# Optimization experiments

Hardware: AMD Instinct MI355X
Metric: run time of the kernel (lower is better)

The kernel has to match this reference:

```python
import jax, jax.numpy as jnp
import numpy as np

B, T, D, H, L, VOC = 2, 2048, 512, 8, 4, 32000
SLOTS = [16384, 8192, 4096]  # base_slots=16384, halved per level
KTOP = 4


def setup_inputs() -> dict:
    key = jax.random.key(0)
    ks = jax.random.split(key, 20)

    def n(i, shape, scale=0.02):
        return jax.random.normal(ks[i], shape, jnp.float32) * scale

    inp = {
        'input_ids': jax.random.randint(ks[0], (B, T), 0, VOC),
        'tok_embed': n(1, (VOC, D)),
        'pos_embed': n(2, (T, D)),
        'Wqkv': n(3, (L, 3 * D, D)), 'bqkv': jnp.zeros((L, 3 * D), jnp.float32),
        'Wo': n(4, (L, D, D)), 'bo': jnp.zeros((L, D), jnp.float32),
        'ln1_s': jnp.ones((L, D), jnp.float32), 'ln1_b': jnp.zeros((L, D), jnp.float32),
        'W1': n(5, (L, 4 * D, D)), 'b1': jnp.zeros((L, 4 * D), jnp.float32),
        'W2': n(6, (L, D, 4 * D)), 'b2': jnp.zeros((L, D), jnp.float32),
        'ln2_s': jnp.ones((L, D), jnp.float32), 'ln2_b': jnp.zeros((L, D), jnp.float32),
        'Wq': n(7, (D, D)), 'bq': jnp.zeros((D,), jnp.float32),
        'Wrp': n(8, (D, D)), 'brp': jnp.zeros((D,), jnp.float32),
        'lnout_s': jnp.ones((D,), jnp.float32), 'lnout_b': jnp.zeros((D,), jnp.float32),
    }
    # hierarchical memory banks (xavier-ish scale)
    for li, s in enumerate(SLOTS):
        inp[f'K{li}'] = n(10 + li, (s, D), float(1.0 / np.sqrt(D)))
        inp[f'V{li}'] = n(13 + li, (s, D), float(1.0 / np.sqrt(D)))
        inp[f's{li}'] = jnp.zeros((s,), jnp.float32)
    return inp


def _ln(x, s, b):
    m = x.mean(-1, keepdims=True)
    v = jnp.mean((x - m) ** 2, -1, keepdims=True)
    return (x - m) / jnp.sqrt(v + 1e-5) * s + b


def reference(input_ids, tok_embed, pos_embed, Wqkv, bqkv, Wo, bo, ln1_s, ln1_b,
              W1, b1, W2, b2, ln2_s, ln2_b, Wq, bq, Wrp, brp, lnout_s, lnout_b,
              K0, V0, s0, K1, V1, s1, K2, V2, s2):
    hd = D // H
    x = tok_embed[input_ids] + pos_embed[None, :, :]  # [B,T,D]
    for i in range(L):
        qkv = x @ Wqkv[i].T + bqkv[i]
        q, k, v = jnp.split(qkv, 3, -1)
        q = q.reshape(B, T, H, hd)
        k = k.reshape(B, T, H, hd)
        v = v.reshape(B, T, H, hd)
        att = jax.nn.softmax(jnp.einsum('bqhd,bkhd->bhqk', q, k) / np.float32(np.sqrt(hd)), -1)
        o = jnp.einsum('bhqk,bkhd->bqhd', att, v).reshape(B, T, D)
        x = _ln(x + (o @ Wo[i].T + bo[i]), ln1_s[i], ln1_b[i])
        f = jax.nn.gelu(x @ W1[i].T + b1[i], approximate=False) @ W2[i].T + b2[i]
        x = _ln(x + f, ln2_s[i], ln2_b[i])
    # hierarchical memory read (top-k gather attention per level)
    qm = x @ Wq.T + bq
    inv_sqrt_d = np.float32(1.0 / np.sqrt(D))
    read = jnp.zeros_like(x)
    for (K, V, sal) in ((K0, V0, s0), (K1, V1, s1), (K2, V2, s2)):
        scores = jnp.einsum('btd,sd->bts', qm, K) * inv_sqrt_d + sal  # [B,T,S]
        ts, ti = jax.lax.top_k(scores, KTOP)
        a = jax.nn.softmax(ts, -1)                 # [B,T,k]
        read = read + jnp.einsum('btk,btkd->btd', a, V[ti])  # gather + reduce
    read = read / np.float32(len(SLOTS))           # uniform level weights 1/num_levels
    x = x + (read @ Wrp.T + brp)
    x = _ln(x, lnout_s, lnout_b)
    return x @ tok_embed.T                          # tied lm_head [B,T,VOC]
```

## Files before the change

### kernel.cpp

```cpp
#include <hip/hip_runtime.h>
#include <cstdint>

typedef __bf16 bf16_t;
typedef __bf16 bf16x2 __attribute__((ext_vector_type(2)));
typedef __bf16 bf16x4 __attribute__((ext_vector_type(4)));
typedef __bf16 bf16x8 __attribute__((ext_vector_type(8)));
typedef float f32x4 __attribute__((ext_vector_type(4)));
typedef unsigned short u16;
typedef unsigned int u32;
typedef unsigned short u16x8 __attribute__((ext_vector_type(8)));

#define DEVI static __device__ __forceinline__

DEVI void g2l16(const void* g, void* l) {
  __builtin_amdgcn_global_load_lds((__attribute__((address_space(1))) void*)g,
                                   (__attribute__((address_space(3))) void*)l,
                                   16, 0, 0);
}

DEVI void tki4(u32* k, u32 nk) {
  if (nk <= k[3]) return;
  k[3] = nk;
  if (k[3] > k[2]) { u32 t = k[2]; k[2] = k[3]; k[3] = t; }
  if (k[2] > k[1]) { u32 t = k[1]; k[1] = k[2]; k[2] = t; }
  if (k[1] > k[0]) { u32 t = k[0]; k[0] = k[1]; k[1] = t; }
}

struct F2BArgs {
  const float* s[10];
  bf16_t* d[10];
  int n4[10];
};
__global__ void k_f2b_all(F2BArgs a) {
  const int seg = blockIdx.y;
  const float* __restrict__ in = a.s[seg];
  bf16_t* __restrict__ out = a.d[seg];
  const long n4 = a.n4[seg];
  const long stride = (long)gridDim.x * blockDim.x;
  for (long i = (long)blockIdx.x * blockDim.x + threadIdx.x; i < n4; i += stride) {
    float4 v = ((const float4*)in)[i];
    bf16x4 o = {(bf16_t)v.x, (bf16_t)v.y, (bf16_t)v.z, (bf16_t)v.w};
    ((bf16x4*)out)[i] = o;
  }
}

__global__ void k_embed(const int* __restrict__ ids, const float* __restrict__ tok,
                        const float* __restrict__ pos, float* __restrict__ x,
                        bf16_t* __restrict__ xb) {
  int r = blockIdx.x;
  int t = r & 2047;
  long id = ids[r];
  int d = threadIdx.x * 2;
  float2 a = *(const float2*)(tok + id * 512 + d);
  float2 p = *(const float2*)(pos + (long)t * 512 + d);
  float o0 = a.x + p.x, o1 = a.y + p.y;
  *(float2*)(x + (long)r * 512 + d) = make_float2(o0, o1);
  bf16x2 ob = {(bf16_t)o0, (bf16_t)o1};
  *(bf16x2*)(xb + (long)r * 512 + d) = ob;
}

DEVI float gelu_f(float f) {
  return 0.5f * f * (1.0f + erff(f * 0.70710678118654752f));
}

template <typename CT, bool BIAS, int EPI>
__global__ __launch_bounds__(256, 2) void k_gemm_bt(
    const bf16_t* __restrict__ A, int lda, const bf16_t* __restrict__ B, int ldb,
    CT* __restrict__ C, int ldc, const float* __restrict__ bias, int K, float alpha,
    bf16_t* __restrict__ qh, bf16_t* __restrict__ kh, bf16_t* __restrict__ vt) {
  __shared__ bf16_t As[4096];
  __shared__ bf16_t Bs[4096];
  const int tid = threadIdx.x;
  const int lane = tid & 63;
  const int w = tid >> 6;
  const int wm = w >> 1, wn = w & 1;
  const int m0 = blockIdx.y * 128;
  const int n0 = blockIdx.x * 128;

  f32x4 acc[4][4];
#pragma unroll
  for (int m = 0; m < 4; ++m)
#pragma unroll
    for (int n = 0; n < 4; ++n) acc[m][n] = (f32x4){0.f, 0.f, 0.f, 0.f};

  const int srow = tid >> 2;
  const int scol = ((tid & 3) ^ ((srow >> 1) & 3)) * 8;
  const int fr = lane & 15;
  const int g4 = lane >> 4;
  const int kg = g4 * 8;

  for (int k0 = 0; k0 < K; k0 += 32) {
#pragma unroll
    for (int p = 0; p < 2; ++p) {
      g2l16(A + (long long)(m0 + p * 64 + srow) * lda + (k0 + scol), As + p * 2048 + w * 512);
      g2l16(B + (long long)(n0 + p * 64 + srow) * ldb + (k0 + scol), Bs + p * 2048 + w * 512);
    }
    __syncthreads();
    bf16x8 fa[4], fb[4];
#pragma unroll
    for (int m = 0; m < 4; ++m) {
      const int row = wm * 64 + m * 16 + fr;
      fa[m] = *(const bf16x8*)(As + row * 32 + (kg ^ (((row >> 1) & 3) << 3)));
    }
#pragma unroll
    for (int n = 0; n < 4; ++n) {
      const int row = wn * 64 + n * 16 + fr;
      fb[n] = *(const bf16x8*)(Bs + row * 32 + (kg ^ (((row >> 1) & 3) << 3)));
    }
#pragma unroll
    for (int m = 0; m < 4; ++m)
#pragma unroll
      for (int n = 0; n < 4; ++n)
        acc[m][n] = __builtin_amdgcn_mfma_f32_16x16x32_bf16(fa[m], fb[n], acc[m][n], 0, 0, 0);
    __syncthreads();
  }

#pragma unroll
  for (int n = 0; n < 4; ++n) {
    const int col = n0 + wn * 64 + n * 16 + fr;
    const float bv = BIAS ? bias[col] : 0.0f;
    if (EPI == 1) {
      const int reg = col >> 9;
      const int h = (col >> 6) & 7;
      const int hd = col & 63;
#pragma unroll
      for (int m = 0; m < 4; ++m) {
        const int rb = m0 + wm * 64 + m * 16 + g4 * 4;
#pragma unroll
        for (int r = 0; r < 4; ++r) {
          const int row = rb + r;
          const int b = row >> 11, t = row & 2047;
          const long long bh = (long long)b * 8 + h;
          float v = acc[m][n][r] + bv;
          if (reg == 0) qh[(bh * 2048 + t) * 64 + hd] = (bf16_t)(v * 0.125f);
          else if (reg == 1) kh[(bh * 2048 + t) * 64 + hd] = (bf16_t)v;
          else vt[(bh * 64 + hd) * 2048 + t] = (bf16_t)v;
        }
      }
    } else {
#pragma unroll
      for (int m = 0; m < 4; ++m) {
        const long long rb = m0 + wm * 64 + m * 16 + g4 * 4;
#pragma unroll
        for (int r = 0; r < 4; ++r) {
          float v = (acc[m][n][r] + bv) * alpha;
          if (EPI == 2) v = gelu_f(v);
          C[(rb + r) * (long long)ldc + col] = (CT)v;
        }
      }
    }
  }
}

template <typename CT, bool BIAS>
__global__ __launch_bounds__(256, 4) void k_gemm64(
    const bf16_t* __restrict__ A, int lda, const bf16_t* __restrict__ B, int ldb,
    CT* __restrict__ C, int ldc, long long sCz, const float* __restrict__ bias,
    int K, float alpha) {
  __shared__ bf16_t As[64 * 32];
  __shared__ bf16_t Bs[128 * 32];
  const int tid = threadIdx.x;
  const int lane = tid & 63;
  const int w = tid >> 6;
  const int wm = w >> 1, wn = w & 1;
  const int m0 = blockIdx.y * 64;
  const int n0 = blockIdx.x * 128;
  const int kz = blockIdx.z;
  A += (long long)kz * K;
  B += (long long)kz * K;
  C += (long long)kz * sCz;

  f32x4 acc[2][4];
#pragma unroll
  for (int m = 0; m < 2; ++m)
#pragma unroll
    for (int n = 0; n < 4; ++n) acc[m][n] = (f32x4){0.f, 0.f, 0.f, 0.f};

  const int srow = tid >> 2;
  const int scol = ((tid & 3) ^ ((srow >> 1) & 3)) * 8;
  const int fr = lane & 15;
  const int g4 = lane >> 4;
  const int kg = g4 * 8;

  for (int k0 = 0; k0 < K; k0 += 32) {
    g2l16(A + (long long)(m0 + srow) * lda + (k0 + scol), As + tid * 8);
    g2l16(B + (long long)(n0 + srow) * ldb + (k0 + scol), Bs + tid * 8);
    g2l16(B + (long long)(n0 + 64 + srow) * ldb + (k0 + scol), Bs + 2048 + tid * 8);
    __syncthreads();
    bf16x8 fa[2], fb[4];
#pragma unroll
    for (int m = 0; m < 2; ++m) {
      const int row = wm * 32 + m * 16 + fr;
      fa[m] = *(const bf16x8*)(As + row * 32 + (kg ^ (((row >> 1) & 3) << 3)));
    }
#pragma unroll
    for (int n = 0; n < 4; ++n) {
      const int row = wn * 64 + n * 16 + fr;
      fb[n] = *(const bf16x8*)(Bs + row * 32 + (kg ^ (((row >> 1) & 3) << 3)));
    }
#pragma unroll
    for (int m = 0; m < 2; ++m)
#pragma unroll
      for (int n = 0; n < 4; ++n)
        acc[m][n] = __builtin_amdgcn_mfma_f32_16x16x32_bf16(fa[m], fb[n], acc[m][n], 0, 0, 0);
    __syncthreads();
  }

#pragma unroll
  for (int n = 0; n < 4; ++n) {
    const int col = n0 + wn * 64 + n * 16 + fr;
    const float bv = (BIAS && kz == 0) ? bias[col] : 0.0f;
#pragma unroll
    for (int m = 0; m < 2; ++m) {
      const long long rb = m0 + wm * 32 + m * 16 + g4 * 4;
#pragma unroll
      for (int r = 0; r < 4; ++r)
        C[(rb + r) * (long long)ldc + col] = (CT)((acc[m][n][r] + bv) * alpha);
    }
  }
}

template <typename CT, int EPI>
__global__ __launch_bounds__(512, 2) void k_gemm256(
    const bf16_t* __restrict__ A, int lda, const bf16_t* __restrict__ B, int ldb,
    CT* __restrict__ C, int ldc, int K, float alpha,
    const float* __restrict__ s0, const float* __restrict__ s1,
    const float* __restrict__ s2, u32* __restrict__ cand) {
  __shared__ char lds[131072];
  const int tid = threadIdx.x;
  const int lane = tid & 63;
  const int w = tid >> 6;
  const int wm = w >> 2, wn = w & 3;
  const int fr = lane & 15;
  const int g4 = lane >> 4;

  const int ny = gridDim.y;
  const int nwg = gridDim.x * ny;
  int orig = blockIdx.y * gridDim.x + blockIdx.x;
  int lin = ((nwg & 7) == 0) ? ((orig & 7) * (nwg >> 3) + (orig >> 3)) : orig;
  const int m0 = (lin % ny) * 256;
  const int n0 = (lin / ny) * 256;

  f32x4 acc[8][4];
#pragma unroll
  for (int m = 0; m < 8; ++m)
#pragma unroll
    for (int n = 0; n < 4; ++n) acc[m][n] = (f32x4){0.f, 0.f, 0.f, 0.f};

  const int sr = tid >> 2;
  const int sc = (tid & 3) * 16;
  const int NT = K >> 6;

  auto stage = [&](int t, int p, int buf) {
    const long long kb = (long long)t * 128 + p * 64;
    char* ab = (char*)lds + buf * 65536 + p * 16384;
    char* bb = ab + 32768;
    const int sw = ((sr >> 1) & 3) << 4;
    g2l16((const char*)A + (long long)(m0 + sr) * (lda * 2) + kb + (sc ^ sw), ab + tid * 16);
    g2l16((const char*)A + (long long)(m0 + 128 + sr) * (lda * 2) + kb + (sc ^ sw),
          ab + (tid + 512) * 16);
    g2l16((const char*)B + (long long)(n0 + sr) * (ldb * 2) + kb + (sc ^ sw), bb + tid * 16);
    g2l16((const char*)B + (long long)(n0 + 128 + sr) * (ldb * 2) + kb + (sc ^ sw),
          bb + (tid + 512) * 16);
  };

  stage(0, 0, 0);
  stage(0, 1, 0);
  asm volatile("s_waitcnt vmcnt(4)" ::: "memory");
  __builtin_amdgcn_s_barrier();
  __builtin_amdgcn_sched_barrier(0);

  int cur = 0;
  for (int t = 0; t < NT; ++t) {
#pragma unroll
    for (int p = 0; p < 2; ++p) {
      const char* ab = (const char*)lds + cur * 65536 + p * 16384;
      const char* bb = ab + 32768;
      bf16x8 fa[8], fb[4];
#pragma unroll
      for (int m = 0; m < 8; ++m) {
        const int row = wm * 128 + m * 16 + fr;
        fa[m] = *(const bf16x8*)(ab + row * 64 + ((g4 * 16) ^ (((row >> 1) & 3) << 4)));
      }
#pragma unroll
      for (int n = 0; n < 4; ++n) {
        const int row = wn * 64 + n * 16 + fr;
        fb[n] = *(const bf16x8*)(bb + row * 64 + ((g4 * 16) ^ (((row >> 1) & 3) << 4)));
      }
      if (t + 1 < NT) stage(t + 1, p, cur ^ 1);
      if (t == NT - 1 && p == 0) {
        asm volatile("s_waitcnt vmcnt(0)" ::: "memory");
      } else {
        asm volatile("s_waitcnt vmcnt(4)" ::: "memory");
      }
      __builtin_amdgcn_s_barrier();
      __builtin_amdgcn_sched_barrier(0);
      __builtin_amdgcn_s_setprio(1);
#pragma unroll
      for (int m = 0; m < 8; ++m)
#pragma unroll
        for (int n = 0; n < 4; ++n)
          acc[m][n] = __builtin_amdgcn_mfma_f32_16x16x32_bf16(fa[m], fb[n], acc[m][n], 0, 0, 0);
      __builtin_amdgcn_s_setprio(0);
    }
    cur ^= 1;
  }

  if (EPI == 0) {
#pragma unroll
    for (int n = 0; n < 4; ++n) {
      const int col = n0 + wn * 64 + n * 16 + fr;
#pragma unroll
      for (int m = 0; m < 8; ++m) {
        const long long rb = m0 + wm * 128 + m * 16 + g4 * 4;
#pragma unroll
        for (int r = 0; r < 4; ++r)
          C[(rb + r) * (long long)ldc + col] = (CT)(acc[m][n][r] * alpha);
      }
    }
  } else {
    const float* salp;
    if (n0 < 16384) salp = s0 + n0;
    else if (n0 < 24576) salp = s1 + (n0 - 16384);
    else salp = s2 + (n0 - 24576);
    float bv[4];
    int coll[4];
#pragma unroll
    for (int n = 0; n < 4; ++n) {
      coll[n] = wn * 64 + n * 16 + fr;
      bv[n] = salp[coll[n]];
    }
    __syncthreads();
    u16* slab = (u16*)lds;
#pragma unroll
    for (int m = 0; m < 8; ++m) {
#pragma unroll
      for (int r = 0; r < 4; ++r) {
        const int rl = wm * 128 + m * 16 + g4 * 4 + r;
        const int sw = (rl & 7) << 3;
#pragma unroll
        for (int n = 0; n < 4; ++n) {
          bf16_t bvv = (bf16_t)(acc[m][n][r] + bv[n]);
          slab[rl * 256 + (coll[n] ^ sw)] = __builtin_bit_cast(u16, bvv);
        }
      }
    }
    __syncthreads();
    const int rr = tid & 255;
    const int hh = tid >> 8;
    const int sw = (rr & 7) << 3;
    u32 rk[4] = {0u, 0u, 0u, 0u};
    const u32 ibase = 0x7FFFu - (u32)n0;
#pragma unroll
    for (int j = 0; j < 16; ++j) {
      const int c0 = hh * 128 + j * 8;
      u16x8 vv = *(const u16x8*)(slab + rr * 256 + (c0 ^ sw));
#pragma unroll
      for (int e = 0; e < 8; ++e) {
        u16 sb = vv[e];
        u32 k16 = (u32)sb ^ (0x8000u | (0x7FFFu * (u32)(sb >> 15)));
        tki4(rk, (k16 << 15) | (ibase - (u32)(c0 + e)));
      }
    }
    __syncthreads();
    u32* res = (u32*)lds;
#pragma unroll
    for (int j = 0; j < 4; ++j) res[(rr * 2 + hh) * 4 + j] = rk[j];
    __syncthreads();
    if (tid < 256) {
      const u32* rp = res + tid * 8;
      u32 fin[4] = {rp[0], rp[1], rp[2], rp[3]};
      tki4(fin, rp[4]); tki4(fin, rp[5]); tki4(fin, rp[6]); tki4(fin, rp[7]);
      u32* cp = cand + ((long long)(m0 + tid) * 112 + (n0 >> 8)) * 4;
#pragma unroll
      for (int j = 0; j < 4; ++j) cp[j] = fin[j];
    }
  }
}

__global__ __launch_bounds__(256, 2) void k_flash(
    const bf16_t* __restrict__ qh, const bf16_t* __restrict__ kh,
    const bf16_t* __restrict__ vt, bf16_t* __restrict__ out) {
  __shared__ bf16_t Ks[2][128 * 64];
  __shared__ bf16_t Vs[2][64 * 128];
  __shared__ bf16_t Ps[4 * 16 * 128];
  const int tid = threadIdx.x;
  const int lane = tid & 63;
  const int w = tid >> 6;
  const int bh = blockIdx.y;
  const int q0 = blockIdx.x * 64;
  const int fr = lane & 15;
  const int g4 = lane >> 4;
  const int kg = g4 * 8;

  bf16x8 qf[2];
  {
    const bf16_t* qb = qh + ((long long)bh * 2048 + q0 + w * 16) * 64;
#pragma unroll
    for (int ks = 0; ks < 2; ++ks)
      qf[ks] = *(const bf16x8*)(qb + fr * 64 + ks * 32 + kg);
  }

  f32x4 oacc[4];
#pragma unroll
  for (int n = 0; n < 4; ++n) oacc[n] = (f32x4){0.f, 0.f, 0.f, 0.f};
  float li[4] = {0.f, 0.f, 0.f, 0.f};

  char* PsW = (char*)(Ps + w * 16 * 128);
  const bf16_t* kbase = kh + (long long)bh * 2048 * 64;
  const bf16_t* vbase = vt + (long long)bh * 64 * 2048;

  auto stage = [&](int kt, int buf) {
#pragma unroll
    for (int i = 0; i < 4; ++i) {
      int row = (w * 4 + i) * 8 + (lane >> 3);
      int c = lane & 7;
      g2l16(kbase + ((long long)(kt * 128 + row)) * 64 + (c ^ (row & 7)) * 8,
            Ks[buf] + (w * 4 + i) * 512);
      int d = w * 16 + i * 4 + (lane >> 4);
      int c2 = lane & 15;
      g2l16(vbase + (long long)d * 2048 + kt * 128 + ((c2 ^ (d & 7)) * 8),
            Vs[buf] + (w * 16 + i * 4) * 128);
    }
  };

  stage(0, 0);
  int buf = 0;
  for (int kt = 0; kt < 16; ++kt) {
    __syncthreads();
    if (kt + 1 < 16) stage(kt + 1, buf ^ 1);

    f32x4 s[8];
#pragma unroll
    for (int n = 0; n < 8; ++n) s[n] = (f32x4){0.f, 0.f, 0.f, 0.f};
#pragma unroll
    for (int ks = 0; ks < 2; ++ks) {
#pragma unroll
      for (int n = 0; n < 8; ++n) {
        int row = n * 16 + fr;
        bf16x8 kf = *(const bf16x8*)((const char*)Ks[buf] + row * 128 +
                                     ((ks * 64 + kg * 2) ^ ((row & 7) << 4)));
        s[n] = __builtin_amdgcn_mfma_f32_16x16x32_bf16(qf[ks], kf, s[n], 0, 0, 0);
      }
    }

#pragma unroll
    for (int r = 0; r < 4; ++r) {
      const int lr = g4 * 4 + r;
      const int sw = (lr & 7) << 4;
      float rs = 0.f;
#pragma unroll
      for (int n = 0; n < 8; ++n) {
        float p = __expf(s[n][r]);
        rs += p;
        *(bf16_t*)(PsW + lr * 256 + (((n * 16 + fr) * 2) ^ sw)) = (bf16_t)p;
      }
      li[r] += rs;
    }

#pragma unroll
    for (int ks = 0; ks < 4; ++ks) {
      bf16x8 pa = *(const bf16x8*)(PsW + fr * 256 +
                                   ((ks * 64 + kg * 2) ^ ((fr & 7) << 4)));
#pragma unroll
      for (int n = 0; n < 4; ++n) {
        int d = n * 16 + fr;
        bf16x8 vf = *(const bf16x8*)((const char*)Vs[buf] + d * 256 +
                                     ((ks * 64 + kg * 2) ^ ((d & 7) << 4)));
        oacc[n] = __builtin_amdgcn_mfma_f32_16x16x32_bf16(pa, vf, oacc[n], 0, 0, 0);
      }
    }
    buf ^= 1;
  }

#pragma unroll
  for (int r = 0; r < 4; ++r) {
    li[r] += __shfl_xor(li[r], 1);
    li[r] += __shfl_xor(li[r], 2);
    li[r] += __shfl_xor(li[r], 4);
    li[r] += __shfl_xor(li[r], 8);
  }

  const int b = bh >> 3, h = bh & 7;
  bf16_t* ob = out + ((long long)b * 2048 + q0 + w * 16) * 512 + h * 64;
#pragma unroll
  for (int r = 0; r < 4; ++r) {
    float inv = 1.0f / li[r];
#pragma unroll
    for (int n = 0; n < 4; ++n)
      ob[(g4 * 4 + r) * 512 + n * 16 + fr] = (bf16_t)(oacc[n][r] * inv);
  }
}

__global__ void k_ln2(const float* __restrict__ xin, const float* __restrict__ d1,
                      const float* __restrict__ d2, const float* __restrict__ s,
                      const float* __restrict__ b, float* __restrict__ xout,
                      bf16_t* __restrict__ xbf) {
  __shared__ float red[8];
  const int r = blockIdx.x;
  const int tid = threadIdx.x;
  const int d = tid * 2;
  const int lane = tid & 63, w = tid >> 6;
  float2 xi = *(const float2*)(xin + (long)r * 512 + d);
  float2 e1 = *(const float2*)(d1 + (long)r * 512 + d);
  float2 e2 = *(const float2*)(d2 + (long)r * 512 + d);
  float y0 = xi.x + e1.x + e2.x, y1 = xi.y + e1.y + e2.y;
  float sum = y0 + y1, ss = y0 * y0 + y1 * y1;
#pragma unroll
  for (int o = 32; o > 0; o >>= 1) { sum += __shfl_xor(sum, o); ss += __shfl_xor(ss, o); }
  if (lane == 0) { red[w] = sum; red[4 + w] = ss; }
  __syncthreads();
  sum = red[0] + red[1] + red[2] + red[3];
  ss = red[4] + red[5] + red[6] + red[7];
  const float mean = sum * (1.0f / 512.0f);
  const float var = ss * (1.0f / 512.0f) - mean * mean;
  const float rstd = rsqrtf(var + 1e-5f);
  float o0 = (y0 - mean) * rstd * s[d] + b[d];
  float o1 = (y1 - mean) * rstd * s[d + 1] + b[d + 1];
  if (xout) *(float2*)(xout + (long)r * 512 + d) = make_float2(o0, o1);
  bf16x2 ob = {(bf16_t)o0, (bf16_t)o1};
  *(bf16x2*)(xbf + (long)r * 512 + d) = ob;
}

__global__ void k_topk3(const u32* __restrict__ cand, float* __restrict__ tv,
                        int* __restrict__ ti) {
  const int r = blockIdx.x * 4 + (threadIdx.x >> 6);
  const int lane = threadIdx.x & 63;
  const u32* cr = cand + (long long)r * 448;
  int base = 0;
  for (int lev = 0; lev < 3; ++lev) {
    const int cnt = lev == 0 ? 256 : (lev == 1 ? 128 : 64);
    const int coff = lev == 0 ? 0 : (lev == 1 ? 16384 : 24576);
    u32 rk[4] = {0u, 0u, 0u, 0u};
    for (int j = lane; j < cnt; j += 64) tki4(rk, cr[base + j]);
    base += cnt;
#pragma unroll
    for (int dd = 1; dd < 64; dd <<= 1) {
      u32 o[4];
#pragma unroll
      for (int j = 0; j < 4; ++j) o[j] = (u32)__shfl_xor((int)rk[j], dd);
#pragma unroll
      for (int j = 0; j < 4; ++j) tki4(rk, o[j]);
    }
    if (lane == 0) {
      const long o = ((long)lev * 4096 + r) * 4;
#pragma unroll
      for (int j = 0; j < 4; ++j) {
        u32 k16 = rk[j] >> 15;
        u16 b = (k16 & 0x8000u) ? (u16)(k16 ^ 0x8000u) : (u16)(~k16);
        u32 fb = ((u32)b) << 16;
        tv[o + j] = __uint_as_float(fb);
        ti[o + j] = (0x7FFF - (int)(rk[j] & 0x7FFF)) - coff;
      }
    }
  }
}

__global__ void k_read(const float* __restrict__ tv, const int* __restrict__ ti,
                       const float* __restrict__ V0, const float* __restrict__ V1,
                       const float* __restrict__ V2, bf16_t* __restrict__ readb) {
  const int r = blockIdx.x;
  const int d = threadIdx.x * 2;
  float a0 = 0.f, a1 = 0.f;
  const float* Vs[3] = {V0, V1, V2};
  const int smax[3] = {16383, 8191, 4095};
#pragma unroll
  for (int lev = 0; lev < 3; ++lev) {
    const float* tvr = tv + ((long)lev * 4096 + r) * 4;
    const int* tir = ti + ((long)lev * 4096 + r) * 4;
    float t0 = tvr[0], t1 = tvr[1], t2 = tvr[2], t3 = tvr[3];
    float m = fmaxf(fmaxf(t0, t1), fmaxf(t2, t3));
    float e0 = __expf(t0 - m), e1 = __expf(t1 - m), e2 = __expf(t2 - m), e3 = __expf(t3 - m);
    float inv = 1.0f / (e0 + e1 + e2 + e3);
    float w4[4] = {e0 * inv, e1 * inv, e2 * inv, e3 * inv};
#pragma unroll
    for (int k = 0; k < 4; ++k) {
      int idx = tir[k];
      idx = idx < 0 ? 0 : (idx > smax[lev] ? smax[lev] : idx);
      const float* vr = Vs[lev] + (long)idx * 512;
      a0 += w4[k] * vr[d];
      a1 += w4[k] * vr[d + 1];
    }
  }
  bf16x2 o = {(bf16_t)(a0 * (1.0f / 3.0f)), (bf16_t)(a1 * (1.0f / 3.0f))};
  *(bf16x2*)(readb + (long)r * 512 + d) = o;
}

extern "C" void kernel_launch(void* const* d_in, const int* in_sizes, int n_in,
                              void* d_out, int out_size, void* d_ws, size_t ws_size,
                              hipStream_t stream) {
  (void)in_sizes; (void)n_in; (void)out_size; (void)ws_size;
  const int* ids = (const int*)d_in[0];
  const float* tok = (const float*)d_in[1];
  const float* pos = (const float*)d_in[2];
  const float* Wqkv = (const float*)d_in[3];
  const float* bqkv = (const float*)d_in[4];
  const float* Wo = (const float*)d_in[5];
  const float* bo = (const float*)d_in[6];
  const float* ln1s = (const float*)d_in[7];
  const float* ln1b = (const float*)d_in[8];
  const float* W1 = (const float*)d_in[9];
  const float* b1 = (const float*)d_in[10];
  const float* W2 = (const float*)d_in[11];
  const float* b2 = (const float*)d_in[12];
  const float* ln2s = (const float*)d_in[13];
  const float* ln2b = (const float*)d_in[14];
  const float* Wq = (const float*)d_in[15];
  const float* bq = (const float*)d_in[16];
  const float* Wrp = (const float*)d_in[17];
  const float* brp = (const float*)d_in[18];
  const float* lnos = (const float*)d_in[19];
  const float* lnob = (const float*)d_in[20];
  const float* K0 = (const float*)d_in[21];
  const float* V0 = (const float*)d_in[22];
  const float* s0 = (const float*)d_in[23];
  const float* K1 = (const float*)d_in[24];
  const float* V1 = (const float*)d_in[25];
  const float* s1 = (const float*)d_in[26];
  const float* K2 = (const float*)d_in[27];
  const float* V2 = (const float*)d_in[28];
  const float* s2 = (const float*)d_in[29];

  char* wp = (char*)d_ws;
  auto walloc = [&](size_t bytes) -> char* {
    char* p = wp; wp += (bytes + 255) & ~(size_t)255; return p;
  };
  char* op = (char*)d_out;
  auto oalloc = [&](size_t bytes) -> char* {
    char* p = op; op += (bytes + 255) & ~(size_t)255; return p;
  };

  bf16_t* Wqkvb = (bf16_t*)oalloc(3145728ULL * 2);
  bf16_t* Wob   = (bf16_t*)oalloc(1048576ULL * 2);
  bf16_t* W1b   = (bf16_t*)oalloc(4194304ULL * 2);
  bf16_t* W2b   = (bf16_t*)oalloc(4194304ULL * 2);
  bf16_t* Wqb   = (bf16_t*)oalloc(262144ULL * 2);
  bf16_t* Wrpb  = (bf16_t*)oalloc(262144ULL * 2);
  bf16_t* Kb    = (bf16_t*)oalloc(28672ULL * 512 * 2);
  bf16_t* hb    = (bf16_t*)oalloc(4096ULL * 2048 * 2);
  u32*    cand  = (u32*)oalloc(4096ULL * 112 * 4 * 4);
  float*  delta = (float*)oalloc(2ULL * 4096 * 512 * 4);

  bf16_t* tokb = (bf16_t*)walloc(16384000ULL * 2);
  float*  x    = (float*)walloc(4096ULL * 512 * 4);
  bf16_t* xb   = (bf16_t*)walloc(4096ULL * 512 * 2);
  bf16_t* qh   = (bf16_t*)walloc(2097152ULL * 2);
  bf16_t* kh   = (bf16_t*)walloc(2097152ULL * 2);
  bf16_t* vt   = (bf16_t*)walloc(2097152ULL * 2);
  bf16_t* attob = (bf16_t*)walloc(4096ULL * 512 * 2);
  bf16_t* qmb  = (bf16_t*)walloc(4096ULL * 512 * 2);
  bf16_t* readb = (bf16_t*)walloc(4096ULL * 512 * 2);
  float*  tval = (float*)walloc(3ULL * 4096 * 4 * 4);
  int*    tidx = (int*)walloc(3ULL * 4096 * 4 * 4);
  bf16_t* xfb  = (bf16_t*)walloc(4096ULL * 512 * 2);

  F2BArgs fa;
  fa.s[0] = tok;  fa.d[0] = tokb;  fa.n4[0] = 4096000;
  fa.s[1] = Wqkv; fa.d[1] = Wqkvb; fa.n4[1] = 786432;
  fa.s[2] = Wo;   fa.d[2] = Wob;   fa.n4[2] = 262144;
  fa.s[3] = W1;   fa.d[3] = W1b;   fa.n4[3] = 1048576;
  fa.s[4] = W2;   fa.d[4] = W2b;   fa.n4[4] = 1048576;
  fa.s[5] = Wq;   fa.d[5] = Wqb;   fa.n4[5] = 65536;
  fa.s[6] = Wrp;  fa.d[6] = Wrpb;  fa.n4[6] = 65536;
  fa.s[7] = K0;   fa.d[7] = Kb;                fa.n4[7] = 2097152;
  fa.s[8] = K1;   fa.d[8] = Kb + 8388608L;     fa.n4[8] = 1048576;
  fa.s[9] = K2;   fa.d[9] = Kb + 12582912L;    fa.n4[9] = 524288;
  k_f2b_all<<<dim3(128, 10), 256, 0, stream>>>(fa);

  k_embed<<<4096, 256, 0, stream>>>(ids, tok, pos, x, xb);

  const long long sCz = 4096LL * 512;
  for (int i = 0; i < 4; ++i) {
    k_gemm_bt<bf16_t, true, 1><<<dim3(12, 32), 256, 0, stream>>>(
        xb, 512, Wqkvb + (long long)i * 786432, 512, (bf16_t*)nullptr, 0,
        bqkv + i * 1536, 512, 1.0f, qh, kh, vt);
    k_flash<<<dim3(32, 16), 256, 0, stream>>>(qh, kh, vt, attob);
    k_gemm64<float, true><<<dim3(4, 64, 2), 256, 0, stream>>>(
        attob, 512, Wob + (long long)i * 262144, 512, delta, 512, sCz,
        bo + i * 512, 256, 1.0f);
    k_ln2<<<4096, 256, 0, stream>>>(x, delta, delta + sCz,
                                    ln1s + i * 512, ln1b + i * 512, x, xb);
    k_gemm_bt<bf16_t, true, 2><<<dim3(16, 32), 256, 0, stream>>>(
        xb, 512, W1b + (long long)i * 1048576, 512, hb, 2048,
        b1 + i * 2048, 512, 1.0f, nullptr, nullptr, nullptr);
    k_gemm64<float, true><<<dim3(4, 64, 2), 256, 0, stream>>>(
        hb, 2048, W2b + (long long)i * 1048576, 2048, delta, 512, sCz,
        b2 + i * 512, 1024, 1.0f);
    k_ln2<<<4096, 256, 0, stream>>>(x, delta, delta + sCz,
                                    ln2s + i * 512, ln2b + i * 512, x, xb);
  }

  k_gemm64<bf16_t, true><<<dim3(4, 64, 1), 256, 0, stream>>>(
      xb, 512, Wqb, 512, qmb, 512, 0LL, bq, 512, 0.044194173824159216f);
  k_gemm256<bf16_t, 1><<<dim3(112, 16), 512, 0, stream>>>(
      qmb, 512, Kb, 512, (bf16_t*)nullptr, 0, 512, 1.0f, s0, s1, s2, cand);
  k_topk3<<<1024, 256, 0, stream>>>(cand, tval, tidx);
  k_read<<<4096, 256, 0, stream>>>(tval, tidx, V0, V1, V2, readb);
  k_gemm64<float, true><<<dim3(4, 64, 2), 256, 0, stream>>>(
      readb, 512, Wrpb, 512, delta, 512, sCz, brp, 256, 1.0f);
  k_ln2<<<4096, 256, 0, stream>>>(x, delta, delta + sCz, lnos, lnob, nullptr, xfb);
  k_gemm256<float, 0><<<dim3(125, 16), 512, 0, stream>>>(
      xfb, 512, tokb, 512, (float*)d_out, 32000, 512, 1.0f,
      nullptr, nullptr, nullptr, nullptr);
}
```

Measured before the change: 1.170 ms.

## Multi-buffer LDS and prefetch two K-tiles ahead in GEMM kernels

Replaces the single-buffered load-sync-compute loop in the 128x128 and 64x128 GEMM kernels with a 4-slot and 3-slot LDS ring. Global-to-LDS loads for tile k+2 are issued while tile k is consumed, using explicit vmcnt waits and one barrier per iteration instead of two, and MFMA priority is raised. This is meant to hide global memory latency behind MFMA work. In exchange it uses more LDS (64KB for the 128x128 kernel), which may lower occupancy under the launch bounds of 2 blocks per CU. It also relies on hand-counted vmcnt values being correct.

```diff
diff --git a/kernel.cpp b/kernel.cpp
--- a/kernel.cpp
+++ b/kernel.cpp
@@ -68,8 +68,8 @@
     const bf16_t* __restrict__ A, int lda, const bf16_t* __restrict__ B, int ldb,
     CT* __restrict__ C, int ldc, const float* __restrict__ bias, int K, float alpha,
     bf16_t* __restrict__ qh, bf16_t* __restrict__ kh, bf16_t* __restrict__ vt) {
-  __shared__ bf16_t As[4096];
-  __shared__ bf16_t Bs[4096];
+  __shared__ bf16_t As[4][4096];
+  __shared__ bf16_t Bs[4][4096];
   const int tid = threadIdx.x;
   const int lane = tid & 63;
   const int w = tid >> 6;
@@ -88,31 +88,55 @@
   const int fr = lane & 15;
   const int g4 = lane >> 4;
   const int kg = g4 * 8;
-
-  for (int k0 = 0; k0 < K; k0 += 32) {
-#pragma unroll
-    for (int p = 0; p < 2; ++p) {
-      g2l16(A + (long long)(m0 + p * 64 + srow) * lda + (k0 + scol), As + p * 2048 + w * 512);
-      g2l16(B + (long long)(n0 + p * 64 + srow) * ldb + (k0 + scol), Bs + p * 2048 + w * 512);
-    }
-    __syncthreads();
+  const int NT = K >> 5;
+
+  auto stage = [&](int kp) {
+    const int slot = kp & 3;
+    bf16_t* as = As[slot];
+    bf16_t* bs = Bs[slot];
+    const int k0 = kp * 32;
+    g2l16(A + (long long)(m0 + srow) * lda + (k0 + scol), as + tid * 8);
+    g2l16(A + (long long)(m0 + 64 + srow) * lda + (k0 + scol), as + 2048 + tid * 8);
+    g2l16(B + (long long)(n0 + srow) * ldb + (k0 + scol), bs + tid * 8);
+    g2l16(B + (long long)(n0 + 64 + srow) * ldb + (k0 + scol), bs + 2048 + tid * 8);
+  };
+
+  stage(0);
+  stage(1);
+  asm volatile("s_waitcnt vmcnt(4)" ::: "memory");
+  __builtin_amdgcn_s_barrier();
+  __builtin_amdgcn_sched_barrier(0);
+
+  for (int k = 0; k < NT; ++k) {
+    const int slot = k & 3;
+    const bf16_t* as = As[slot];
+    const bf16_t* bs = Bs[slot];
     bf16x8 fa[4], fb[4];
 #pragma unroll
     for (int m = 0; m < 4; ++m) {
       const int row = wm * 64 + m * 16 + fr;
-      fa[m] = *(const bf16x8*)(As + row * 32 + (kg ^ (((row >> 1) & 3) << 3)));
+      fa[m] = *(const bf16x8*)(as + row * 32 + (kg ^ (((row >> 1) & 3) << 3)));
     }
 #pragma unroll
     for (int n = 0; n < 4; ++n) {
       const int row = wn * 64 + n * 16 + fr;
-      fb[n] = *(const bf16x8*)(Bs + row * 32 + (kg ^ (((row >> 1) & 3) << 3)));
-    }
+      fb[n] = *(const bf16x8*)(bs + row * 32 + (kg ^ (((row >> 1) & 3) << 3)));
+    }
+    if (k + 2 < NT) stage(k + 2);
+    if (k < NT - 2) {
+      asm volatile("s_waitcnt vmcnt(4)" ::: "memory");
+    } else {
+      asm volatile("s_waitcnt vmcnt(0)" ::: "memory");
+    }
+    __builtin_amdgcn_s_barrier();
+    __builtin_amdgcn_sched_barrier(0);
+    __builtin_amdgcn_s_setprio(1);
 #pragma unroll
     for (int m = 0; m < 4; ++m)
 #pragma unroll
       for (int n = 0; n < 4; ++n)
         acc[m][n] = __builtin_amdgcn_mfma_f32_16x16x32_bf16(fa[m], fb[n], acc[m][n], 0, 0, 0);
-    __syncthreads();
+    __builtin_amdgcn_s_setprio(0);
   }
 
 #pragma unroll
@@ -157,8 +181,8 @@
     const bf16_t* __restrict__ A, int lda, const bf16_t* __restrict__ B, int ldb,
     CT* __restrict__ C, int ldc, long long sCz, const float* __restrict__ bias,
     int K, float alpha) {
-  __shared__ bf16_t As[64 * 32];
-  __shared__ bf16_t Bs[128 * 32];
+  __shared__ bf16_t As[3][2048];
+  __shared__ bf16_t Bs[3][4096];
   const int tid = threadIdx.x;
   const int lane = tid & 63;
   const int w = tid >> 6;
@@ -181,29 +205,54 @@
   const int fr = lane & 15;
   const int g4 = lane >> 4;
   const int kg = g4 * 8;
-
-  for (int k0 = 0; k0 < K; k0 += 32) {
-    g2l16(A + (long long)(m0 + srow) * lda + (k0 + scol), As + tid * 8);
-    g2l16(B + (long long)(n0 + srow) * ldb + (k0 + scol), Bs + tid * 8);
-    g2l16(B + (long long)(n0 + 64 + srow) * ldb + (k0 + scol), Bs + 2048 + tid * 8);
-    __syncthreads();
+  const int NT = K >> 5;
+
+  auto stage = [&](int kp) {
+    const int slot = kp % 3;
+    bf16_t* as = As[slot];
+    bf16_t* bs = Bs[slot];
+    const int k0 = kp * 32;
+    g2l16(A + (long long)(m0 + srow) * lda + (k0 + scol), as + tid * 8);
+    g2l16(B + (long long)(n0 + srow) * ldb + (k0 + scol), bs + tid * 8);
+    g2l16(B + (long long)(n0 + 64 + srow) * ldb + (k0 + scol), bs + 2048 + tid * 8);
+  };
+
+  stage(0);
+  stage(1);
+  asm volatile("s_waitcnt vmcnt(3)" ::: "memory");
+  __builtin_amdgcn_s_barrier();
+  __builtin_amdgcn_sched_barrier(0);
+
+  for (int k = 0; k < NT; ++k) {
+    const int slot = k % 3;
+    const bf16_t* as = As[slot];
+    const bf16_t* bs = Bs[slot];
     bf16x8 fa[2], fb[4];
 #pragma unroll
     for (int m = 0; m < 2; ++m) {
       const int row = wm * 32 + m * 16 + fr;
-      fa[m] = *(const bf16x8*)(As + row * 32 + (kg ^ (((row >> 1) & 3) << 3)));
+      fa[m] = *(const bf16x8*)(as + row * 32 + (kg ^ (((row >> 1) & 3) << 3)));
     }
 #pragma unroll
     for (int n = 0; n < 4; ++n) {
       const int row = wn * 64 + n * 16 + fr;
-      fb[n] = *(const bf16x8*)(Bs + row * 32 + (kg ^ (((row >> 1) & 3) << 3)));
-    }
+      fb[n] = *(const bf16x8*)(bs + row * 32 + (kg ^ (((row >> 1) & 3) << 3)));
+    }
+    if (k + 2 < NT) stage(k + 2);
+    if (k < NT - 2) {
+      asm volatile("s_waitcnt vmcnt(3)" ::: "memory");
+    } else {
+      asm volatile("s_waitcnt vmcnt(0)" ::: "memory");
+    }
+    __builtin_amdgcn_s_barrier();
+    __builtin_amdgcn_sched_barrier(0);
+    __builtin_amdgcn_s_setprio(1);
 #pragma unroll
     for (int m = 0; m < 2; ++m)
 #pragma unroll
       for (int n = 0; n < 4; ++n)
         acc[m][n] = __builtin_amdgcn_mfma_f32_16x16x32_bf16(fa[m], fb[n], acc[m][n], 0, 0, 0);
-    __syncthreads();
+    __builtin_amdgcn_s_setprio(0);
   }
 
 #pragma unroll
```

Result: faster. 1.143 ms (-2.3%).
